# Performance work log

Hardware: AMD Instinct MI355X
Metric: run time of the kernel (lower is better)

Reference implementation:

```python
import jax, jax.numpy as jnp
import numpy as np

D_MODEL = 2048
STATE = 16
KCONV = 4
EXPAND = 2
D_INNER = D_MODEL * EXPAND
EPS = 1e-05


def setup_inputs() -> dict:
    key = jax.random.key(0)
    ks = jax.random.split(key, 10)
    s = 0.02
    x = jax.random.normal(ks[0], (2, 2048, D_MODEL), dtype=jnp.float32)
    norm_w = jnp.ones((D_MODEL,), jnp.float32)
    in_proj_w = jax.random.normal(ks[1], (D_INNER * 2, D_MODEL), jnp.float32) * s
    conv_w = jax.random.normal(ks[2], (D_INNER, 1, KCONV), jnp.float32) * s  # depthwise (O,I/g,K)
    conv_b = jnp.zeros((D_INNER,), jnp.float32)
    x_proj_w = jax.random.normal(ks[3], (STATE * 2 + 1, D_INNER), jnp.float32) * s
    dt_w = jax.random.normal(ks[4], (D_INNER, 1), jnp.float32) * s
    dt_b = jnp.zeros((D_INNER,), jnp.float32)
    A_log = jnp.log(jnp.broadcast_to(jnp.arange(1, STATE + 1, dtype=jnp.float32)[None, :], (D_INNER, STATE)))
    D_param = jnp.ones((D_INNER,), jnp.float32)
    out_proj_w = jax.random.normal(ks[5], (D_MODEL, D_INNER), jnp.float32) * s
    return {"x": x, "norm_w": norm_w, "in_proj_w": in_proj_w, "conv_w": conv_w,
            "conv_b": conv_b, "x_proj_w": x_proj_w, "dt_w": dt_w, "dt_b": dt_b,
            "A_log": A_log, "D_param": D_param, "out_proj_w": out_proj_w}


def _silu(v):
    return v * jax.nn.sigmoid(v)


def reference(x, norm_w, in_proj_w, conv_w, conv_b, x_proj_w, dt_w, dt_b, A_log, D_param, out_proj_w):
    residual = x
    # RMSNorm
    xn = x * jax.lax.rsqrt(jnp.mean(x * x, axis=-1, keepdims=True) + EPS) * norm_w
    # in_proj -> split into x_inner, z
    xz = jnp.einsum('bld,ed->ble', xn, in_proj_w)  # [B,L,2*d_inner]
    x_inner, z = jnp.split(xz, 2, axis=-1)
    # causal depthwise conv1d (torch pads K-1 both sides then truncates to L == left pad only)
    xc = jnp.transpose(x_inner, (0, 2, 1))  # [B,d_inner,L]
    xc = jax.lax.conv_general_dilated(
        xc, conv_w, window_strides=(1,), padding=[(KCONV - 1, 0)],
        dimension_numbers=('NCH', 'OIH', 'NCH'), feature_group_count=D_INNER)
    xc = xc + conv_b[None, :, None]
    xc = _silu(jnp.transpose(xc, (0, 2, 1)))  # [B,L,d_inner]
    # SSM parameter projections
    x_ssm = jnp.einsum('bld,ed->ble', xc, x_proj_w)  # [B,L,2N+1]
    dt = jax.nn.softplus(x_ssm[..., -1:] * dt_w[:, 0] + dt_b)  # [B,L,d_inner]
    B_p = x_ssm[..., :STATE]            # [B,L,N]
    C_p = x_ssm[..., STATE:2 * STATE]   # [B,L,N]
    A = -jnp.exp(A_log)                 # [d_inner,N]

    batch = x.shape[0]
    h0 = jnp.zeros((batch, D_INNER, STATE), x.dtype)

    def step(h, inp):
        dt_t, B_t, C_t, u_t = inp  # [B,d_inner],[B,N],[B,N],[B,d_inner]
        dA = jnp.exp(dt_t[..., None] * A)  # [B,d_inner,N]
        h = dA * h + (dt_t * u_t)[..., None] * B_t[:, None, :]
        y_t = jnp.sum(h * C_t[:, None, :], axis=-1) + D_param * u_t
        return h, y_t

    seq_first = lambda a: jnp.swapaxes(a, 0, 1)
    _, ys = jax.lax.scan(step, h0, (seq_first(dt), seq_first(B_p), seq_first(C_p), seq_first(xc)))
    y = jnp.swapaxes(ys, 0, 1)  # [B,L,d_inner]
    y = y * _silu(z)
    return jnp.einsum('ble,de->bld', y, out_proj_w) + residual
```

## Files before the change

kernel.cpp:

```cpp
#include <hip/hip_runtime.h>

#define NTOK   4096
#define LSEQ   2048
#define DMODEL 2048
#define DINNER 4096
#define NSTATE 16
#define NCHAIN 8192

using short8 = __attribute__((ext_vector_type(8))) short;
using f32x4  = __attribute__((ext_vector_type(4))) float;

__device__ inline float b2f(short s) {
    union { unsigned u; float f; } v;
    v.u = ((unsigned)(unsigned short)s) << 16;
    return v.f;
}
__device__ inline short f2b(float f) {
    unsigned u = __float_as_uint(f);
    unsigned r = (u + 0x7fffu + ((u >> 16) & 1u)) >> 16;
    return (short)r;
}

template <int OFF>
__device__ inline float swz(float v) {
    return __int_as_float(__builtin_amdgcn_ds_swizzle(__float_as_int(v), OFF));
}
template <int CTRL>
__device__ inline float qperm(float v) {
    return __int_as_float(
        __builtin_amdgcn_mov_dpp(__float_as_int(v), CTRL, 0xF, 0xF, true));
}
__device__ inline float ror8(float v) {
    return __int_as_float(
        __builtin_amdgcn_mov_dpp(__float_as_int(v), 0x128, 0xF, 0xF, true));
}

__global__ __launch_bounds__(256) void f32_to_bf16_kernel(
    const float* __restrict__ in, short* __restrict__ out, int n8) {
    int i = blockIdx.x * 256 + threadIdx.x;
    if (i >= n8) return;
    const float4* p = (const float4*)in + 2 * (size_t)i;
    float4 a = p[0], b = p[1];
    short8 s;
    s[0] = f2b(a.x); s[1] = f2b(a.y); s[2] = f2b(a.z); s[3] = f2b(a.w);
    s[4] = f2b(b.x); s[5] = f2b(b.y); s[6] = f2b(b.z); s[7] = f2b(b.w);
    *(short8*)(out + 8 * (size_t)i) = s;
}

__global__ __launch_bounds__(256) void rmsnorm_kernel(
    const float* __restrict__ x, const float* __restrict__ w,
    short* __restrict__ xn) {
    const int t = blockIdx.x, tid = threadIdx.x;
    const float4* xr = (const float4*)(x + (size_t)t * DMODEL + tid * 8);
    float4 a = xr[0], b = xr[1];
    float v[8] = {a.x, a.y, a.z, a.w, b.x, b.y, b.z, b.w};
    float ss = 0.f;
#pragma unroll
    for (int j = 0; j < 8; ++j) ss += v[j] * v[j];
#pragma unroll
    for (int o = 32; o > 0; o >>= 1) ss += __shfl_down(ss, o, 64);
    __shared__ float sred[4];
    if ((tid & 63) == 0) sred[tid >> 6] = ss;
    __syncthreads();
    float r = rsqrtf((sred[0] + sred[1] + sred[2] + sred[3]) * (1.f / DMODEL) + 1e-5f);
    const float4* wr = (const float4*)(w + tid * 8);
    float4 wa = wr[0], wb = wr[1];
    float wv[8] = {wa.x, wa.y, wa.z, wa.w, wb.x, wb.y, wb.z, wb.w};
    short8 o8;
#pragma unroll
    for (int j = 0; j < 8; ++j) o8[j] = f2b(v[j] * r * wv[j]);
    *(short8*)(xn + (size_t)t * DMODEL + tid * 8) = o8;
}

template <bool ADD_RES, bool F32OUT, bool SPLIT>
__global__ __launch_bounds__(256) void gemm_bt(
    const short* __restrict__ A, const short* __restrict__ B,
    const float* __restrict__ RES, void* __restrict__ Cp, void* __restrict__ Cp2,
    int M, int N, int K) {
    __shared__ __align__(16) short As[128 * 32];
    __shared__ __align__(16) short Bs[128 * 32];

    const int tid  = threadIdx.x;
    const int wave = tid >> 6;
    const int lane = tid & 63;
    const int lr   = lane & 15;
    const int q    = lane >> 4;
    const int m0   = blockIdx.x * 128;
    const int n0   = blockIdx.y * 128;
    const int wm   = (wave >> 1) * 64;
    const int wn   = (wave & 1) * 64;

    f32x4 acc[4][4] = {};

    for (int k0 = 0; k0 < K; k0 += 32) {
#pragma unroll
        for (int p = 0; p < 2; ++p) {
            int i16 = p * 256 + tid;
            int row = i16 >> 2, ch = i16 & 3;
            const short* ga = A + (size_t)(m0 + row) * K + k0 + ch * 8;
            const short* gb = B + (size_t)(n0 + row) * K + k0 + ch * 8;
            __builtin_amdgcn_global_load_lds(
                (const __attribute__((address_space(1))) void*)ga,
                (__attribute__((address_space(3))) void*)((char*)As + i16 * 16),
                16, 0, 0);
            __builtin_amdgcn_global_load_lds(
                (const __attribute__((address_space(1))) void*)gb,
                (__attribute__((address_space(3))) void*)((char*)Bs + i16 * 16),
                16, 0, 0);
        }
        __syncthreads();

        short8 af[4], bfr[4];
#pragma unroll
        for (int i = 0; i < 4; ++i) {
            af[i]  = *(const short8*)&As[(wm + i * 16 + lr) * 32 + q * 8];
            bfr[i] = *(const short8*)&Bs[(wn + i * 16 + lr) * 32 + q * 8];
        }
#pragma unroll
        for (int i = 0; i < 4; ++i)
#pragma unroll
            for (int j = 0; j < 4; ++j)
                acc[i][j] = __builtin_amdgcn_mfma_f32_16x16x32_bf16(
                    af[i], bfr[j], acc[i][j], 0, 0, 0);
        __syncthreads();
    }

    short* sdst = nullptr;
    int    noff = 0;
    if (SPLIT) {
        bool hi = (n0 >= DINNER);
        sdst = hi ? (short*)Cp2 : (short*)Cp;
        noff = hi ? DINNER : 0;
    }

#pragma unroll
    for (int i = 0; i < 4; ++i)
#pragma unroll
        for (int j = 0; j < 4; ++j)
#pragma unroll
            for (int r = 0; r < 4; ++r) {
                int m = m0 + wm + i * 16 + q * 4 + r;
                int n = n0 + wn + j * 16 + lr;
                float v = acc[i][j][r];
                if (SPLIT) {
                    sdst[(size_t)m * DINNER + (n - noff)] = f2b(v);
                } else {
                    size_t idx = (size_t)m * N + n;
                    if (ADD_RES) v += RES[idx];
                    if (F32OUT) ((float*)Cp)[idx] = v;
                    else        ((short*)Cp)[idx] = f2b(v);
                }
            }
}

__global__ __launch_bounds__(256) void conv_silu_t_kernel(
    const short* __restrict__ xi, const float* __restrict__ cw,
    const float* __restrict__ cb, short* __restrict__ xc,
    short* __restrict__ uT) {
    __shared__ short tin[67][72];
    __shared__ short tout[64][72];
    const int bb = blockIdx.z;
    const int l0 = blockIdx.x * 64;
    const int c0 = blockIdx.y * 64;
    const int tid = threadIdx.x;

    for (int idx = tid; idx < 67 * 8; idx += 256) {
        int row = idx >> 3, cs = (idx & 7) * 8;
        int ls = l0 - 3 + row;
        short8 v;
        if (ls >= 0) {
            v = *(const short8*)(xi + ((size_t)(bb * LSEQ + ls)) * DINNER + c0 + cs);
        } else {
#pragma unroll
            for (int j = 0; j < 8; ++j) v[j] = 0;
        }
        *(short8*)&tin[row][cs] = v;
    }
    __syncthreads();

    const int r    = tid >> 2;
    const int cb16 = (tid & 3) * 16;
    short8 a[4][2];
#pragma unroll
    for (int k = 0; k < 4; ++k) {
        a[k][0] = *(const short8*)&tin[r + k][cb16];
        a[k][1] = *(const short8*)&tin[r + k][cb16 + 8];
    }
    short o16[16];
#pragma unroll
    for (int j = 0; j < 16; ++j) {
        const int c = c0 + cb16 + j;
        float4 w4 = *(const float4*)(cw + (size_t)c * 4);
        float acc = cb[c];
        acc += b2f(a[0][j >> 3][j & 7]) * w4.x;
        acc += b2f(a[1][j >> 3][j & 7]) * w4.y;
        acc += b2f(a[2][j >> 3][j & 7]) * w4.z;
        acc += b2f(a[3][j >> 3][j & 7]) * w4.w;
        o16[j] = f2b(acc / (1.f + __expf(-acc)));
    }
    {
        short8 lo, hi;
#pragma unroll
        for (int j = 0; j < 8; ++j) { lo[j] = o16[j]; hi[j] = o16[8 + j]; }
        short* dst = xc + ((size_t)(bb * LSEQ + l0 + r)) * DINNER + c0 + cb16;
        *(short8*)dst = lo;
        *(short8*)(dst + 8) = hi;
    }
#pragma unroll
    for (int j = 0; j < 16; ++j) tout[r][cb16 + j] = o16[j];
    __syncthreads();

    const int rr = tid >> 3;
    const int l8 = (tid & 7) * 8;
#pragma unroll
    for (int p = 0; p < 2; ++p) {
        int cr = p * 32 + rr;
        short8 v;
#pragma unroll
        for (int j = 0; j < 8; ++j) v[j] = tout[l8 + j][cr];
        *(short8*)(uT + ((size_t)(bb * DINNER + c0 + cr)) * LSEQ + l0 + l8) = v;
    }
}

__global__ __launch_bounds__(256) void xproj_kernel(
    const short* __restrict__ xc, const float* __restrict__ W,
    float* __restrict__ BT, float* __restrict__ CT, float* __restrict__ s32T) {
    const int t0 = blockIdx.x * 2, tid = threadIdx.x;
    float xv0[16], xv1[16];
    {
        short8 a = *(const short8*)(xc + (size_t)t0 * DINNER + tid * 16);
        short8 b = *(const short8*)(xc + (size_t)t0 * DINNER + tid * 16 + 8);
        short8 c = *(const short8*)(xc + (size_t)(t0 + 1) * DINNER + tid * 16);
        short8 d = *(const short8*)(xc + (size_t)(t0 + 1) * DINNER + tid * 16 + 8);
#pragma unroll
        for (int j = 0; j < 8; ++j) {
            xv0[j] = b2f(a[j]); xv0[8 + j] = b2f(b[j]);
            xv1[j] = b2f(c[j]); xv1[8 + j] = b2f(d[j]);
        }
    }
    float acc0[33], acc1[33];
#pragma unroll
    for (int e = 0; e < 33; ++e) {
        const float4* wr = (const float4*)(W + (size_t)e * DINNER + tid * 16);
        float4 w0 = wr[0], w1 = wr[1], w2 = wr[2], w3 = wr[3];
        float wv[16] = {w0.x, w0.y, w0.z, w0.w, w1.x, w1.y, w1.z, w1.w,
                        w2.x, w2.y, w2.z, w2.w, w3.x, w3.y, w3.z, w3.w};
        float s0 = 0.f, s1 = 0.f;
#pragma unroll
        for (int j = 0; j < 16; ++j) { s0 += xv0[j] * wv[j]; s1 += xv1[j] * wv[j]; }
        acc0[e] = s0; acc1[e] = s1;
    }
    __shared__ float red[4][33];
#pragma unroll
    for (int tk = 0; tk < 2; ++tk) {
#pragma unroll
        for (int e = 0; e < 33; ++e) {
            float v = tk ? acc1[e] : acc0[e];
#pragma unroll
            for (int o = 32; o > 0; o >>= 1) v += __shfl_down(v, o, 64);
            if ((tid & 63) == 0) red[tid >> 6][e] = v;
        }
        __syncthreads();
        if (tid < 33) {
            float val = red[0][tid] + red[1][tid] + red[2][tid] + red[3][tid];
            const int t = t0 + tk;
            const int bb = t >> 11, l = t & (LSEQ - 1);
            if (tid < 16)
                BT[((size_t)bb * NSTATE + tid) * LSEQ + l] = val;
            else if (tid < 32)
                CT[((size_t)bb * NSTATE + (tid - 16)) * LSEQ + l] = val;
            else
                s32T[(size_t)bb * LSEQ + l] = val;
        }
        __syncthreads();
    }
}

__global__ __launch_bounds__(256) void dt_kernel(
    const float* __restrict__ s32T, const float* __restrict__ dt_w,
    const float* __restrict__ dt_b, float* __restrict__ dtT0,
    float* __restrict__ dtT1) {
    const int chain = blockIdx.x;
    const int b = chain >> 12;
    const int c = chain & (DINNER - 1);
    const float dtw = dt_w[c], dtb = dt_b[c];
    const float* src = s32T + (size_t)b * LSEQ + threadIdx.x * 8;
    float* dst = (b ? dtT1 : dtT0) + (size_t)c * LSEQ + threadIdx.x * 8;
    float4 s0 = ((const float4*)src)[0], s1 = ((const float4*)src)[1];
    float sv[8] = {s0.x, s0.y, s0.z, s0.w, s1.x, s1.y, s1.z, s1.w};
    float dv[8];
#pragma unroll
    for (int j = 0; j < 8; ++j) {
        float v = sv[j] * dtw + dtb;
        dv[j] = (v > 20.f) ? v : __logf(1.f + __expf(v));
    }
    ((float4*)dst)[0] = make_float4(dv[0], dv[1], dv[2], dv[3]);
    ((float4*)dst)[1] = make_float4(dv[4], dv[5], dv[6], dv[7]);
}

#define GQ 4
__global__ __launch_bounds__(256) void scan_state_kernel(
    const float* __restrict__ BT, const float* __restrict__ CT,
    const float* __restrict__ dtT0, const float* __restrict__ dtT1,
    const short* __restrict__ uT, const short* __restrict__ Z,
    short* __restrict__ yout,
    const float* __restrict__ A_log, const float* __restrict__ D_par) {
    const int tid  = threadIdx.x;
    const int n    = tid & 15;
    const int slot = tid >> 4;
    const int cA   = blockIdx.x * 32 + slot;
    const int cB   = cA + 16;
    const int b    = cA >> 12;
    const int ca   = cA & (DINNER - 1);
    const int cb2  = cB & (DINNER - 1);

    const float AnA = -__expf(A_log[ca * NSTATE + n]);
    const float AnB = -__expf(A_log[cb2 * NSTATE + n]);
    const float DpA = D_par[ca];
    const float DpB = D_par[cb2];

    const float* Bb  = BT + ((size_t)b * NSTATE + n) * LSEQ;
    const float* Cb  = CT + ((size_t)b * NSTATE + n) * LSEQ;
    const float* dbA = (b ? dtT1 : dtT0) + (size_t)ca * LSEQ;
    const float* dbB = (b ? dtT1 : dtT0) + (size_t)cb2 * LSEQ;
    const short* ubA = uT + (size_t)cA * LSEQ;
    const short* ubB = uT + (size_t)cB * LSEQ;
    const short* ueA = ubA + n;
    const short* ueB = ubB + n;
    const short* zpA = Z + ((size_t)b * LSEQ + n) * DINNER + ca;
    const short* zpB = Z + ((size_t)b * LSEQ + n) * DINNER + cb2;
    short*       ypA = yout + ((size_t)b * LSEQ + n) * DINNER + ca;
    short*       ypB = yout + ((size_t)b * LSEQ + n) * DINNER + cb2;

    f32x4 Bq[GQ], Cq[GQ], dqA[GQ], dqB[GQ];
    uint2 uqA[GQ], uqB[GQ];
#pragma unroll
    for (int g = 0; g < GQ; ++g) {
        Bq[g]  = *(const f32x4*)(Bb + g * 4);
        Cq[g]  = *(const f32x4*)(Cb + g * 4);
        dqA[g] = *(const f32x4*)(dbA + g * 4);
        dqB[g] = *(const f32x4*)(dbB + g * 4);
        uqA[g] = *(const uint2*)(ubA + g * 4);
        uqB[g] = *(const uint2*)(ubB + g * 4);
    }

    float hA = 0.f, hB = 0.f;
    for (int l0 = 0; l0 < LSEQ; l0 += 16) {
        const float uA = b2f(ueA[0]), zA = b2f(zpA[0]);
        const float uB = b2f(ueB[0]), zB = b2f(zpB[0]);
        const bool refill = (l0 + 16 < LSEQ);
        float ysA = 0.f, ysB = 0.f;
#pragma unroll
        for (int g = 0; g < GQ; ++g) {
            f32x4 B4 = Bq[g], C4 = Cq[g], dA4 = dqA[g], dB4 = dqB[g];
            uint2 u4A = uqA[g], u4B = uqB[g];
            if (refill) {
                const int lp = l0 + 16 + g * 4;
                Bq[g]  = *(const f32x4*)(Bb + lp);
                Cq[g]  = *(const f32x4*)(Cb + lp);
                dqA[g] = *(const f32x4*)(dbA + lp);
                dqB[g] = *(const f32x4*)(dbB + lp);
                uqA[g] = *(const uint2*)(ubA + lp);
                uqB[g] = *(const uint2*)(ubB + lp);
            }
            float uvA[4], uvB[4], eA[4], eB[4];
#pragma unroll
            for (int i = 0; i < 4; ++i) {
                unsigned wA = (i < 2) ? u4A.x : u4A.y;
                unsigned wB = (i < 2) ? u4B.x : u4B.y;
                union { unsigned uu; float ff; } t0, t1;
                t0.uu = (i & 1) ? (wA & 0xffff0000u) : (wA << 16);
                t1.uu = (i & 1) ? (wB & 0xffff0000u) : (wB << 16);
                uvA[i] = t0.ff; uvB[i] = t1.ff;
                eA[i] = __expf(dA4[i] * AnA);
                eB[i] = __expf(dB4[i] * AnB);
            }
            float pA[4], pB[4];
#pragma unroll
            for (int i = 0; i < 4; ++i) {
                hA = eA[i] * hA + (dA4[i] * uvA[i]) * B4[i];
                pA[i] = hA * C4[i];
            }
#pragma unroll
            for (int i = 0; i < 4; ++i) {
                hB = eB[i] * hB + (dB4[i] * uvB[i]) * B4[i];
                pB[i] = hB * C4[i];
            }
            float tA[4], tB[4];
#pragma unroll
            for (int i = 0; i < 4; ++i) { tA[i] = ror8(pA[i]); tB[i] = ror8(pB[i]); }
#pragma unroll
            for (int i = 0; i < 4; ++i) { pA[i] += tA[i]; pB[i] += tB[i]; }
#pragma unroll
            for (int i = 0; i < 4; ++i) { tA[i] = swz<0x101F>(pA[i]); tB[i] = swz<0x101F>(pB[i]); }
#pragma unroll
            for (int i = 0; i < 4; ++i) { pA[i] += tA[i]; pB[i] += tB[i]; }
#pragma unroll
            for (int i = 0; i < 4; ++i) { pA[i] += qperm<0x4E>(pA[i]); pB[i] += qperm<0x4E>(pB[i]); }
#pragma unroll
            for (int i = 0; i < 4; ++i) { pA[i] += qperm<0xB1>(pA[i]); pB[i] += qperm<0xB1>(pB[i]); }
#pragma unroll
            for (int i = 0; i < 4; ++i) {
                ysA = (n == g * 4 + i) ? pA[i] : ysA;
                ysB = (n == g * 4 + i) ? pB[i] : ysB;
            }
        }
        {
            float yA  = ysA + DpA * uA;
            float zgA = zA / (1.f + __expf(-zA));
            ypA[0] = f2b(yA * zgA);
            float yB  = ysB + DpB * uB;
            float zgB = zB / (1.f + __expf(-zB));
            ypB[0] = f2b(yB * zgB);
        }
        ueA += 16; ueB += 16;
        zpA += (size_t)16 * DINNER; zpB += (size_t)16 * DINNER;
        ypA += (size_t)16 * DINNER; ypB += (size_t)16 * DINNER;
    }
}

extern "C" void kernel_launch(void* const* d_in, const int* in_sizes, int n_in,
                              void* d_out, int out_size, void* d_ws, size_t ws_size,
                              hipStream_t stream) {
    const float* x      = (const float*)d_in[0];
    const float* norm_w = (const float*)d_in[1];
    const float* w_in   = (const float*)d_in[2];
    const float* conv_w = (const float*)d_in[3];
    const float* conv_b = (const float*)d_in[4];
    const float* w_xp   = (const float*)d_in[5];
    const float* dt_w   = (const float*)d_in[6];
    const float* dt_b   = (const float*)d_in[7];
    const float* A_log  = (const float*)d_in[8];
    const float* D_par  = (const float*)d_in[9];
    const float* w_out  = (const float*)d_in[10];
    float* out = (float*)d_out;

    char* ws = (char*)d_ws;
    short* wb   = (short*)(ws);
    short* xn   = (short*)(ws + (size_t)(32 << 20));
    short* Xi   = (short*)(ws + (size_t)(48 << 20));
    short* Zb   = (short*)(ws + (size_t)(80 << 20));
    short* xc   = (short*)(ws + (size_t)(112 << 20));
    float* BT   = (float*)(ws + (size_t)(144 << 20));
    float* CT   = (float*)(ws + (size_t)(144 << 20) + (256 << 10));
    float* s32T = (float*)(ws + (size_t)(144 << 20) + (512 << 10));
    float* dtT0 = (float*)Xi;
    float* dtT1 = out;

    f32_to_bf16_kernel<<<(2 * DINNER * DMODEL / 8) / 256, 256, 0, stream>>>(
        w_in, wb, 2 * DINNER * DMODEL / 8);
    rmsnorm_kernel<<<NTOK, 256, 0, stream>>>(x, norm_w, xn);
    gemm_bt<false, false, true><<<dim3(NTOK / 128, 8192 / 128), 256, 0, stream>>>(
        xn, wb, nullptr, Xi, Zb, NTOK, 2 * DINNER, DMODEL);
    conv_silu_t_kernel<<<dim3(LSEQ / 64, DINNER / 64, 2), 256, 0, stream>>>(
        Xi, conv_w, conv_b, xc, wb);
    xproj_kernel<<<NTOK / 2, 256, 0, stream>>>(xc, w_xp, BT, CT, s32T);
    dt_kernel<<<NCHAIN, 256, 0, stream>>>(s32T, dt_w, dt_b, dtT0, dtT1);
    scan_state_kernel<<<NCHAIN / 32, 256, 0, stream>>>(
        BT, CT, dtT0, dtT1, wb, Zb, xc, A_log, D_par);
    f32_to_bf16_kernel<<<(DMODEL * DINNER / 8) / 256, 256, 0, stream>>>(
        w_out, xn, DMODEL * DINNER / 8);
    gemm_bt<true, true, false><<<dim3(NTOK / 128, DMODEL / 128), 256, 0, stream>>>(
        xc, xn, x, out, nullptr, NTOK, DMODEL, DINNER);
}
```

Before: 1.016 ms.

## Replace in_proj GEMM with 256x256 tiled, double-buffered direct-to-LDS pipelined kernel

Adds a new 512-thread GEMM for the in_proj projection. It uses 256x256 tiles and a K-step of 64, and loads global memory straight into double-buffered LDS with global_load_lds. It XOR-swizzles the LDS layout to avoid bank conflicts, interleaves the staging loads with MFMA quarters, and raises scheduling priority around the MFMAs. The goal is to hide memory latency and raise data reuse in the largest GEMM, at the cost of higher register and LDS use (128 KB of LDS per block). The old SPLIT path is removed from the generic GEMM.

```diff
diff --git a/kernel.cpp b/kernel.cpp
--- a/kernel.cpp
+++ b/kernel.cpp
@@ -72,10 +72,155 @@
     *(short8*)(xn + (size_t)t * DMODEL + tid * 8) = o8;
 }
 
-template <bool ADD_RES, bool F32OUT, bool SPLIT>
+__global__ __launch_bounds__(512, 2) void gemm8_split(
+    const short* __restrict__ A, const short* __restrict__ B,
+    short* __restrict__ Cp, short* __restrict__ Cp2, int K) {
+    __shared__ __align__(16) short Alds[2][256][64];
+    __shared__ __align__(16) short Blds[2][256][64];
+
+    const int tid = threadIdx.x;
+    const int lane = tid & 63;
+    const int lr = lane & 15;
+    const int q2 = lane >> 4;
+    const int w  = tid >> 6;
+    const int wmp = w >> 2;
+    const int wnp = w & 3;
+    const int m0 = blockIdx.x * 256;
+    const int n0 = blockIdx.y * 256;
+    const int NT = K / 64;
+    const int niter = NT / 2;
+
+    f32x4 acc[8][4] = {};
+    short8 Af[4][2];
+    short8 Bf[4][2];
+
+    auto STAGE = [&](int T, int c) {
+        if (T >= NT) return;
+        const int buf = T & 1;
+        const int k0 = T * 64;
+        const bool isA = (c < 2);
+        const int half = c & 1;
+        const short* G = isA ? A : B;
+        const int row0 = isA ? m0 : n0;
+        char* ldsbase = isA ? (char*)&Alds[buf][0][0] : (char*)&Blds[buf][0][0];
+#pragma unroll
+        for (int j = 0; j < 2; ++j) {
+            int r = half * 128 + j * 64 + (tid >> 3);
+            int csrc = ((tid & 7) * 8) ^ ((r & 7) * 8);
+            const short* src = G + (size_t)(row0 + r) * K + k0 + csrc;
+            __builtin_amdgcn_global_load_lds(
+                (const __attribute__((address_space(1))) void*)src,
+                (__attribute__((address_space(3))) void*)(
+                    ldsbase + half * 16384 + j * 8192 + tid * 16),
+                16, 0, 0);
+        }
+    };
+    auto LDA = [&](int buf, int qm) {
+#pragma unroll
+        for (int mf2 = 0; mf2 < 4; ++mf2)
+#pragma unroll
+            for (int ks = 0; ks < 2; ++ks) {
+                int r = wmp * 128 + qm * 64 + mf2 * 16 + lr;
+                int ce = (ks * 32 + q2 * 8) ^ ((lr & 7) << 3);
+                Af[mf2][ks] = *(const short8*)&Alds[buf][r][ce];
+            }
+    };
+    auto LDB = [&](int buf, int qn) {
+#pragma unroll
+        for (int nf2 = 0; nf2 < 2; ++nf2)
+#pragma unroll
+            for (int ks = 0; ks < 2; ++ks) {
+                int r = wnp * 64 + qn * 32 + nf2 * 16 + lr;
+                int ce = (ks * 32 + q2 * 8) ^ ((lr & 7) << 3);
+                Bf[qn * 2 + nf2][ks] = *(const short8*)&Blds[buf][r][ce];
+            }
+    };
+    auto MM = [&](int qm, int qn) {
+        __builtin_amdgcn_s_setprio(1);
+#pragma unroll
+        for (int mf2 = 0; mf2 < 4; ++mf2)
+#pragma unroll
+            for (int nf2 = 0; nf2 < 2; ++nf2)
+#pragma unroll
+                for (int ks = 0; ks < 2; ++ks)
+                    acc[qm * 4 + mf2][qn * 2 + nf2] =
+                        __builtin_amdgcn_mfma_f32_16x16x32_bf16(
+                            Af[mf2][ks], Bf[qn * 2 + nf2][ks],
+                            acc[qm * 4 + mf2][qn * 2 + nf2], 0, 0, 0);
+        __builtin_amdgcn_s_setprio(0);
+    };
+
+#pragma unroll
+    for (int c = 0; c < 4; ++c) STAGE(0, c);
+#pragma unroll
+    for (int c = 0; c < 4; ++c) STAGE(1, c);
+    asm volatile("s_waitcnt vmcnt(8)" ::: "memory");
+    __builtin_amdgcn_sched_barrier(0);
+    __builtin_amdgcn_s_barrier();
+
+    for (int t = 0; t < niter; ++t) {
+        const int T0 = 2 * t;
+        LDA(0, 0); LDB(0, 0);
+        if (t > 0) STAGE(T0 + 1, 1);
+        MM(0, 0);
+        __builtin_amdgcn_s_barrier();
+        LDB(0, 1);
+        if (t > 0) STAGE(T0 + 1, 2);
+        MM(0, 1);
+        __builtin_amdgcn_s_barrier();
+        LDA(0, 1);
+        if (t > 0) STAGE(T0 + 1, 3);
+        MM(1, 0);
+        __builtin_amdgcn_s_barrier();
+        STAGE(T0 + 2, 0);
+        MM(1, 1);
+        if (t + 1 < niter) {
+            asm volatile("s_waitcnt vmcnt(2)" ::: "memory");
+        } else {
+            asm volatile("s_waitcnt vmcnt(0)" ::: "memory");
+        }
+        __builtin_amdgcn_sched_barrier(0);
+        __builtin_amdgcn_s_barrier();
+        LDA(1, 0); LDB(1, 0);
+        STAGE(T0 + 2, 1);
+        MM(0, 0);
+        __builtin_amdgcn_s_barrier();
+        LDB(1, 1);
+        STAGE(T0 + 2, 2);
+        MM(0, 1);
+        __builtin_amdgcn_s_barrier();
+        LDA(1, 1);
+        STAGE(T0 + 2, 3);
+        MM(1, 0);
+        __builtin_amdgcn_s_barrier();
+        STAGE(T0 + 3, 0);
+        MM(1, 1);
+        if (t + 1 < niter) {
+            asm volatile("s_waitcnt vmcnt(2)" ::: "memory");
+            __builtin_amdgcn_sched_barrier(0);
+            __builtin_amdgcn_s_barrier();
+        }
+    }
+
+    const bool hi = (n0 >= DINNER);
+    short* sdst = hi ? Cp2 : Cp;
+    const int noff = hi ? DINNER : 0;
+#pragma unroll
+    for (int mf = 0; mf < 8; ++mf)
+#pragma unroll
+        for (int nf = 0; nf < 4; ++nf)
+#pragma unroll
+            for (int rr2 = 0; rr2 < 4; ++rr2) {
+                int m = m0 + wmp * 128 + mf * 16 + q2 * 4 + rr2;
+                int n = n0 + wnp * 64 + nf * 16 + lr;
+                sdst[(size_t)m * DINNER + (n - noff)] = f2b(acc[mf][nf][rr2]);
+            }
+}
+
+template <bool ADD_RES, bool F32OUT>
 __global__ __launch_bounds__(256) void gemm_bt(
     const short* __restrict__ A, const short* __restrict__ B,
-    const float* __restrict__ RES, void* __restrict__ Cp, void* __restrict__ Cp2,
+    const float* __restrict__ RES, void* __restrict__ Cp,
     int M, int N, int K) {
     __shared__ __align__(16) short As[128 * 32];
     __shared__ __align__(16) short Bs[128 * 32];
@@ -125,14 +270,6 @@
         __syncthreads();
     }
 
-    short* sdst = nullptr;
-    int    noff = 0;
-    if (SPLIT) {
-        bool hi = (n0 >= DINNER);
-        sdst = hi ? (short*)Cp2 : (short*)Cp;
-        noff = hi ? DINNER : 0;
-    }
-
 #pragma unroll
     for (int i = 0; i < 4; ++i)
 #pragma unroll
@@ -141,15 +278,11 @@
             for (int r = 0; r < 4; ++r) {
                 int m = m0 + wm + i * 16 + q * 4 + r;
                 int n = n0 + wn + j * 16 + lr;
+                size_t idx = (size_t)m * N + n;
                 float v = acc[i][j][r];
-                if (SPLIT) {
-                    sdst[(size_t)m * DINNER + (n - noff)] = f2b(v);
-                } else {
-                    size_t idx = (size_t)m * N + n;
-                    if (ADD_RES) v += RES[idx];
-                    if (F32OUT) ((float*)Cp)[idx] = v;
-                    else        ((short*)Cp)[idx] = f2b(v);
-                }
+                if (ADD_RES) v += RES[idx];
+                if (F32OUT) ((float*)Cp)[idx] = v;
+                else        ((short*)Cp)[idx] = f2b(v);
             }
 }
 
@@ -450,8 +583,8 @@
     f32_to_bf16_kernel<<<(2 * DINNER * DMODEL / 8) / 256, 256, 0, stream>>>(
         w_in, wb, 2 * DINNER * DMODEL / 8);
     rmsnorm_kernel<<<NTOK, 256, 0, stream>>>(x, norm_w, xn);
-    gemm_bt<false, false, true><<<dim3(NTOK / 128, 8192 / 128), 256, 0, stream>>>(
-        xn, wb, nullptr, Xi, Zb, NTOK, 2 * DINNER, DMODEL);
+    gemm8_split<<<dim3(NTOK / 256, 8192 / 256), 512, 0, stream>>>(
+        xn, wb, Xi, Zb, DMODEL);
     conv_silu_t_kernel<<<dim3(LSEQ / 64, DINNER / 64, 2), 256, 0, stream>>>(
         Xi, conv_w, conv_b, xc, wb);
     xproj_kernel<<<NTOK / 2, 256, 0, stream>>>(xc, w_xp, BT, CT, s32T);
@@ -460,6 +593,6 @@
         BT, CT, dtT0, dtT1, wb, Zb, xc, A_log, D_par);
     f32_to_bf16_kernel<<<(DMODEL * DINNER / 8) / 256, 256, 0, stream>>>(
         w_out, xn, DMODEL * DINNER / 8);
-    gemm_bt<true, true, false><<<dim3(NTOK / 128, DMODEL / 128), 256, 0, stream>>>(
-        xc, xn, x, out, nullptr, NTOK, DMODEL, DINNER);
-}
+    gemm_bt<true, true><<<dim3(NTOK / 128, DMODEL / 128), 256, 0, stream>>>(
+        xc, xn, x, out, NTOK, DMODEL, DINNER);
+}
```

Result: faster. 955.5 us (-5.9%).
